# Kernel tuning notes

Hardware: AMD Instinct MI355X
Metric: run time of the kernel (lower is better)

## Reference

```python
import jax, jax.numpy as jnp
import numpy as np

B, N, FDIM, REL, H = 4, 256, 256, 16, 8
D = FDIM // H


def setup_inputs() -> dict:
    key = jax.random.key(0)
    ks = jax.random.split(key, 10)
    s_f = 1.0 / np.sqrt(FDIM)
    s_kv = 1.0 / np.sqrt(FDIM + REL)
    return {
        "node_features": jax.random.normal(ks[0], (B, N, FDIM), jnp.float32),
        "relative_positions": jax.random.normal(ks[1], (B, N, N, REL), jnp.float32),
        # torch Linear weights stored transposed -> here [in, out]
        "Wq": jax.random.uniform(ks[2], (FDIM, FDIM), jnp.float32, -s_f, s_f),
        "bq": jax.random.uniform(ks[3], (FDIM,), jnp.float32, -s_f, s_f),
        "Wk": jax.random.uniform(ks[4], (FDIM + REL, FDIM), jnp.float32, -s_kv, s_kv),
        "bk": jax.random.uniform(ks[5], (FDIM,), jnp.float32, -s_kv, s_kv),
        "Wv": jax.random.uniform(ks[6], (FDIM + REL, FDIM), jnp.float32, -s_kv, s_kv),
        "bv": jax.random.uniform(ks[7], (FDIM,), jnp.float32, -s_kv, s_kv),
        "Wo": jax.random.uniform(ks[8], (FDIM, FDIM), jnp.float32, -s_f, s_f),
        "bo": jax.random.uniform(ks[9], (FDIM,), jnp.float32, -s_f, s_f),
    }


def reference(node_features, relative_positions, Wq, bq, Wk, bk, Wv, bv, Wo, bo):
    b, n, f = node_features.shape
    # Q: [b, n_i, H, D]
    Q = (node_features @ Wq + bq).reshape(b, n, H, D)
    # per-edge K/V input: [b, i, j, f+rel] where feature part is node j's features
    nf_j = jnp.broadcast_to(node_features[:, None, :, :], (b, n, n, f))
    kv_in = jnp.concatenate([nf_j, relative_positions], axis=-1)
    K = (kv_in @ Wk + bk).reshape(b, n, n, H, D)  # [b, i, j, h, d]
    V = (kv_in @ Wv + bv).reshape(b, n, n, H, D)
    scale = 1.0 / jnp.sqrt(jnp.asarray(D, node_features.dtype))
    scores = jnp.einsum('bihd,bijhd->bhij', Q, K) * scale
    attn = jax.nn.softmax(scores, axis=-1)
    wv = jnp.einsum('bhij,bijhd->bihd', attn, V).reshape(b, n, f)
    return node_features + (wv @ Wo + bo)
```

## Files before the change

kernel.cpp:

```cpp
#include <hip/hip_runtime.h>


#define BB 4
#define NN 256
#define FD 256
#define RL 16
#define NH 8
#define HD 32

#define OFF_Q    0
#define OFF_KN   (BB*NN*FD)
#define OFF_VN   (OFF_KN + BB*NN*FD/2)

#define ATP 260
#define RLP 20

static __device__ __forceinline__ unsigned short f2bf(float x) {
  unsigned int u = __float_as_uint(x);
  unsigned int r = (u + 0x7fffu + ((u >> 16) & 1u)) >> 16;
  return (unsigned short)r;
}
static __device__ __forceinline__ float bf2f(unsigned short h) {
  return __uint_as_float(((unsigned int)h) << 16);
}
static __device__ __forceinline__ float4 bf4(ushort4 u) {
  return make_float4(bf2f(u.x), bf2f(u.y), bf2f(u.z), bf2f(u.w));
}

__global__ __launch_bounds__(256) void k_qkv5(
    const float* __restrict__ nf,
    const float* __restrict__ Wq, const float* __restrict__ bq,
    const float* __restrict__ Wk, const float* __restrict__ bk,
    const float* __restrict__ Wv, const float* __restrict__ bv,
    float* __restrict__ ws) {
  const int ROWS = 8;
  __shared__ float lrowT[FD][ROWS];
  const int row0 = blockIdx.x * ROWS;
  const int sel  = blockIdx.y;
  const float* W; const float* bias;
  if (sel == 0)      { W = Wq; bias = bq; }
  else if (sel == 1) { W = Wk; bias = bk; }
  else               { W = Wv; bias = bv; }
  const int tid = threadIdx.x;
  {
    float v[ROWS];
    #pragma unroll
    for (int t = 0; t < ROWS; ++t) v[t] = nf[(row0 + t) * FD + tid];
    #pragma unroll
    for (int t = 0; t < ROWS; ++t) lrowT[tid][t] = v[t];
  }
  __syncthreads();
  float acc[ROWS];
  #pragma unroll
  for (int r = 0; r < ROWS; ++r) acc[r] = 0.f;
  #pragma unroll 8
  for (int k = 0; k < FD; ++k) {
    const float w = W[k * FD + tid];
    float4 a0 = *(const float4*)&lrowT[k][0];
    float4 a1 = *(const float4*)&lrowT[k][4];
    acc[0] += a0.x * w; acc[1] += a0.y * w; acc[2] += a0.z * w; acc[3] += a0.w * w;
    acc[4] += a1.x * w; acc[5] += a1.y * w; acc[6] += a1.z * w; acc[7] += a1.w * w;
  }
  const float bb = bias[tid];
  if (sel == 1) {
    const int b2 = row0 >> 8, i0 = row0 & 255;
    unsigned short* kout = (unsigned short*)(ws + OFF_KN) + ((size_t)b2 * FD + tid) * NN + i0;
    ushort4 v0, v1;
    v0.x = f2bf(acc[0] + bb); v0.y = f2bf(acc[1] + bb);
    v0.z = f2bf(acc[2] + bb); v0.w = f2bf(acc[3] + bb);
    v1.x = f2bf(acc[4] + bb); v1.y = f2bf(acc[5] + bb);
    v1.z = f2bf(acc[6] + bb); v1.w = f2bf(acc[7] + bb);
    ((ushort4*)kout)[0] = v0;
    ((ushort4*)kout)[1] = v1;
  } else if (sel == 2) {
    unsigned short* outp = (unsigned short*)(ws + OFF_VN);
    #pragma unroll
    for (int r = 0; r < ROWS; ++r)
      outp[(size_t)(row0 + r) * FD + tid] = f2bf(acc[r] + bb);
  } else {
    float* outp = ws + OFF_Q;
    #pragma unroll
    for (int r = 0; r < ROWS; ++r)
      outp[(row0 + r) * FD + tid] = acc[r] + bb;
  }
}

__global__ __launch_bounds__(256, 2) void k_attn5(
    const float* __restrict__ rel,
    const float* __restrict__ Wk,
    const float* __restrict__ Wv,
    const float* __restrict__ nf,
    const float* __restrict__ Wo,
    const float* __restrict__ bo,
    float* __restrict__ out,
    float* __restrict__ ws) {
  const float* Q = ws + OFF_Q;
  const unsigned short* KnB = (const unsigned short*)(ws + OFF_KN);
  const unsigned short* VnB = (const unsigned short*)(ws + OFF_VN);

  const int bid = (blockIdx.x & 7) * 64 + (blockIdx.x >> 3);
  const int b  = bid >> 7;
  const int i0 = (bid & 127) * 2;
  const int tid = threadIdx.x;
  const int l = tid & 63, w = tid >> 6;

  __shared__ float q[2][FD];
  __shared__ float qrs[2][NH * RL];
  __shared__ float rlds[2 * NN * RLP];
  __shared__ float at[2 * NH * ATP];
  __shared__ float ar[2][NH * RL];
  __shared__ float part[8 * FD];
  __shared__ float wvT[FD * 2];

  const float scale = 0.17677669529663687f;
  q[0][tid] = Q[(b * NN + i0) * FD + tid] * scale;
  q[1][tid] = Q[(b * NN + i0 + 1) * FD + tid] * scale;

  #pragma unroll
  for (int ii = 0; ii < 2; ++ii) {
    const float4* rp = (const float4*)(rel + ((size_t)(b * NN + i0 + ii)) * (NN * RL));
    #pragma unroll
    for (int m = 0; m < 4; ++m) {
      const int idx = tid + 256 * m;
      float4 v = rp[idx];
      *(float4*)&rlds[(ii * NN + (idx >> 2)) * RLP + (idx & 3) * 4] = v;
    }
  }

  {
    const int ii = l >> 5, hh = (l >> 4) & 1, r = l & 15;
    const int h = 2 * w + hh;
    const float* wrow = Wk + (FD + r) * FD + h * HD;
    const float* qq = &q[ii][h * HD];
    float a = 0.f;
    #pragma unroll
    for (int d = 0; d < HD; ++d) a += qq[d] * wrow[d];
    qrs[ii][h * RL + r] = a;
  }
  __syncthreads();

  float s[2][2][4];
  #pragma unroll
  for (int ii = 0; ii < 2; ++ii)
    #pragma unroll
    for (int hh = 0; hh < 2; ++hh)
      #pragma unroll
      for (int jj = 0; jj < 4; ++jj) s[ii][hh][jj] = 0.f;
  {
    const ushort4* kp = (const ushort4*)(KnB + ((size_t)b * FD + 64 * w) * NN) + l;
    #pragma unroll 2
    for (int dd = 0; dd < 8; ++dd) {
      float4 qv00 = *(const float4*)&q[0][64 * w + 4 * dd];
      float4 qv01 = *(const float4*)&q[0][64 * w + 32 + 4 * dd];
      float4 qv10 = *(const float4*)&q[1][64 * w + 4 * dd];
      float4 qv11 = *(const float4*)&q[1][64 * w + 32 + 4 * dd];
      #pragma unroll
      for (int e = 0; e < 4; ++e) {
        float4 k0 = bf4(kp[(4 * dd + e) * (NN / 4)]);
        float4 k1 = bf4(kp[(32 + 4 * dd + e) * (NN / 4)]);
        const float a0 = (&qv00.x)[e], a1 = (&qv01.x)[e];
        const float b0 = (&qv10.x)[e], b1 = (&qv11.x)[e];
        s[0][0][0] += a0 * k0.x; s[0][0][1] += a0 * k0.y;
        s[0][0][2] += a0 * k0.z; s[0][0][3] += a0 * k0.w;
        s[1][0][0] += b0 * k0.x; s[1][0][1] += b0 * k0.y;
        s[1][0][2] += b0 * k0.z; s[1][0][3] += b0 * k0.w;
        s[0][1][0] += a1 * k1.x; s[0][1][1] += a1 * k1.y;
        s[0][1][2] += a1 * k1.z; s[0][1][3] += a1 * k1.w;
        s[1][1][0] += b1 * k1.x; s[1][1][1] += b1 * k1.y;
        s[1][1][2] += b1 * k1.z; s[1][1][3] += b1 * k1.w;
      }
    }
  }

  #pragma unroll
  for (int ii = 0; ii < 2; ++ii) {
    float4 qa0 = *(const float4*)&qrs[ii][(2 * w) * RL + 0];
    float4 qa1 = *(const float4*)&qrs[ii][(2 * w) * RL + 4];
    float4 qa2 = *(const float4*)&qrs[ii][(2 * w) * RL + 8];
    float4 qa3 = *(const float4*)&qrs[ii][(2 * w) * RL + 12];
    float4 qb0 = *(const float4*)&qrs[ii][(2 * w + 1) * RL + 0];
    float4 qb1 = *(const float4*)&qrs[ii][(2 * w + 1) * RL + 4];
    float4 qb2 = *(const float4*)&qrs[ii][(2 * w + 1) * RL + 8];
    float4 qb3 = *(const float4*)&qrs[ii][(2 * w + 1) * RL + 12];
    #pragma unroll
    for (int jj = 0; jj < 4; ++jj) {
      const float* rv = &rlds[(ii * NN + 4 * l + jj) * RLP];
      float4 r0 = *(const float4*)&rv[0];
      float4 r1 = *(const float4*)&rv[4];
      float4 r2 = *(const float4*)&rv[8];
      float4 r3 = *(const float4*)&rv[12];
      s[ii][0][jj] += qa0.x*r0.x + qa0.y*r0.y + qa0.z*r0.z + qa0.w*r0.w
                    + qa1.x*r1.x + qa1.y*r1.y + qa1.z*r1.z + qa1.w*r1.w
                    + qa2.x*r2.x + qa2.y*r2.y + qa2.z*r2.z + qa2.w*r2.w
                    + qa3.x*r3.x + qa3.y*r3.y + qa3.z*r3.z + qa3.w*r3.w;
      s[ii][1][jj] += qb0.x*r0.x + qb0.y*r0.y + qb0.z*r0.z + qb0.w*r0.w
                    + qb1.x*r1.x + qb1.y*r1.y + qb1.z*r1.z + qb1.w*r1.w
                    + qb2.x*r2.x + qb2.y*r2.y + qb2.z*r2.z + qb2.w*r2.w
                    + qb3.x*r3.x + qb3.y*r3.y + qb3.z*r3.z + qb3.w*r3.w;
    }
  }

  #pragma unroll
  for (int ii = 0; ii < 2; ++ii) {
    #pragma unroll
    for (int hh = 0; hh < 2; ++hh) {
      float v = fmaxf(fmaxf(s[ii][hh][0], s[ii][hh][1]),
                      fmaxf(s[ii][hh][2], s[ii][hh][3]));
      #pragma unroll
      for (int off = 32; off; off >>= 1) v = fmaxf(v, __shfl_xor(v, off));
      float4 p;
      p.x = __expf(s[ii][hh][0] - v); p.y = __expf(s[ii][hh][1] - v);
      p.z = __expf(s[ii][hh][2] - v); p.w = __expf(s[ii][hh][3] - v);
      float sum = p.x + p.y + p.z + p.w;
      #pragma unroll
      for (int off = 32; off; off >>= 1) sum += __shfl_xor(sum, off);
      const float rec = 1.f / sum;
      p.x *= rec; p.y *= rec; p.z *= rec; p.w *= rec;
      *(float4*)&at[(ii * NH + 2 * w + hh) * ATP + 4 * l] = p;
    }
  }

  #pragma unroll
  for (int ii = 0; ii < 2; ++ii) {
    const int r = l & 15, sl = l >> 4;
    const int h = 2 * w + (sl & 1);
    const int jb = (sl >> 1) * 128;
    const float* atp = at + (ii * NH + h) * ATP + jb;
    const float* rlp = rlds + (ii * NN + jb) * RLP + r;
    float a = 0.f;
    #pragma unroll 4
    for (int jj = 0; jj < 128; ++jj) a += atp[jj] * rlp[jj * RLP];
    a += __shfl_xor(a, 32);
    if (l < 32) ar[ii][32 * w + l] = a;
  }
  __syncthreads();

  {
    const int h = l >> 3;
    const ushort4* vp = (const ushort4*)(VnB + (size_t)b * NN * FD) + l;
    const float* ap0 = at + h * ATP + 64 * w;
    const float* ap1 = at + (NH + h) * ATP + 64 * w;
    float4 a0 = make_float4(0,0,0,0), a1 = make_float4(0,0,0,0);
    #pragma unroll 4
    for (int jj = 0; jj < 64; ++jj) {
      float4 v = bf4(vp[(64 * w + jj) * (FD / 4)]);
      float p0 = ap0[jj], p1 = ap1[jj];
      a0.x += p0*v.x; a0.y += p0*v.y; a0.z += p0*v.z; a0.w += p0*v.w;
      a1.x += p1*v.x; a1.y += p1*v.y; a1.z += p1*v.z; a1.w += p1*v.w;
    }
    ((float4*)part)[w * 64 + l]       = a0;
    ((float4*)part)[(4 + w) * 64 + l] = a1;
  }
  __syncthreads();

  {
    const int c = tid, h2 = c >> 5;
    float s0 = part[c] + part[FD + c] + part[2*FD + c] + part[3*FD + c];
    float s1 = part[4*FD + c] + part[5*FD + c] + part[6*FD + c] + part[7*FD + c];
    #pragma unroll
    for (int r = 0; r < RL; ++r) {
      const float wvr = Wv[(FD + r) * FD + c];
      s0 += ar[0][h2 * RL + r] * wvr;
      s1 += ar[1][h2 * RL + r] * wvr;
    }
    *(float2*)&wvT[2 * c] = make_float2(s0, s1);
  }
  __syncthreads();

  {
    const int c = tid;
    float acc0 = 0.f, acc1 = 0.f;
    #pragma unroll 4
    for (int k4 = 0; k4 < FD / 4; ++k4) {
      float4 wa = *(const float4*)&wvT[8 * k4];
      float4 wb = *(const float4*)&wvT[8 * k4 + 4];
      float w0 = Wo[(4 * k4 + 0) * FD + c];
      float w1 = Wo[(4 * k4 + 1) * FD + c];
      float w2 = Wo[(4 * k4 + 2) * FD + c];
      float w3 = Wo[(4 * k4 + 3) * FD + c];
      acc0 += wa.x * w0 + wa.z * w1 + wb.x * w2 + wb.z * w3;
      acc1 += wa.y * w0 + wa.w * w1 + wb.y * w2 + wb.w * w3;
    }
    const float bb = bo[c];
    out[(b * NN + i0) * FD + c]     = nf[(b * NN + i0) * FD + c]     + acc0 + bb;
    out[(b * NN + i0 + 1) * FD + c] = nf[(b * NN + i0 + 1) * FD + c] + acc1 + bb;
  }
}

extern "C" void kernel_launch(void* const* d_in, const int* in_sizes, int n_in,
                              void* d_out, int out_size, void* d_ws, size_t ws_size,
                              hipStream_t stream) {
  const float* nf  = (const float*)d_in[0];
  const float* rel = (const float*)d_in[1];
  const float* Wq  = (const float*)d_in[2];
  const float* bq  = (const float*)d_in[3];
  const float* Wk  = (const float*)d_in[4];
  const float* bk  = (const float*)d_in[5];
  const float* Wv  = (const float*)d_in[6];
  const float* bv  = (const float*)d_in[7];
  const float* Wo  = (const float*)d_in[8];
  const float* bo  = (const float*)d_in[9];
  float* out = (float*)d_out;
  float* ws  = (float*)d_ws;

  k_qkv5 <<<dim3(BB * NN / 8, 3), 256, 0, stream>>>(nf, Wq, bq, Wk, bk, Wv, bv, ws);
  k_attn5<<<BB * NN / 2, 256, 0, stream>>>(rel, Wk, Wv, nf, Wo, bo, out, ws);
}
```

Measured before the change: 41.61 us.

## Double threads per block, split-K QKV projection, transpose rel layout, bf16 Wo

```diff
diff --git a/kernel.cpp b/kernel.cpp
--- a/kernel.cpp
+++ b/kernel.cpp
@@ -11,9 +11,10 @@
 #define OFF_Q    0
 #define OFF_KN   (BB*NN*FD)
 #define OFF_VN   (OFF_KN + BB*NN*FD/2)
+#define OFF_WO   (OFF_VN + BB*NN*FD/2)
 
 #define ATP 260
-#define RLP 20
+#define RLT 262
 
 static __device__ __forceinline__ unsigned short f2bf(float x) {
   unsigned int u = __float_as_uint(x);
@@ -23,80 +24,101 @@
 static __device__ __forceinline__ float bf2f(unsigned short h) {
   return __uint_as_float(((unsigned int)h) << 16);
 }
-static __device__ __forceinline__ float4 bf4(ushort4 u) {
-  return make_float4(bf2f(u.x), bf2f(u.y), bf2f(u.z), bf2f(u.w));
-}
-
-__global__ __launch_bounds__(256) void k_qkv5(
+
+__global__ __launch_bounds__(512) void k_qkv6(
     const float* __restrict__ nf,
     const float* __restrict__ Wq, const float* __restrict__ bq,
     const float* __restrict__ Wk, const float* __restrict__ bk,
     const float* __restrict__ Wv, const float* __restrict__ bv,
+    const float* __restrict__ Wo,
     float* __restrict__ ws) {
-  const int ROWS = 8;
-  __shared__ float lrowT[FD][ROWS];
-  const int row0 = blockIdx.x * ROWS;
-  const int sel  = blockIdx.y;
+  const int tid = threadIdx.x;
+  const int sel = blockIdx.y;
+  if (sel == 3) {
+    if (tid < 256) {
+      const int k2 = blockIdx.x;
+      unsigned int lo = f2bf(Wo[(2 * k2) * FD + tid]);
+      unsigned int hi = f2bf(Wo[(2 * k2 + 1) * FD + tid]);
+      ((unsigned int*)(ws + OFF_WO))[k2 * FD + tid] = lo | (hi << 16);
+    }
+    return;
+  }
+  __shared__ __align__(16) float lrowT[FD * 12];
+  const int row0 = blockIdx.x * 8;
   const float* W; const float* bias;
   if (sel == 0)      { W = Wq; bias = bq; }
   else if (sel == 1) { W = Wk; bias = bk; }
   else               { W = Wv; bias = bv; }
-  const int tid = threadIdx.x;
-  {
-    float v[ROWS];
-    #pragma unroll
-    for (int t = 0; t < ROWS; ++t) v[t] = nf[(row0 + t) * FD + tid];
-    #pragma unroll
-    for (int t = 0; t < ROWS; ++t) lrowT[tid][t] = v[t];
-  }
-  __syncthreads();
-  float acc[ROWS];
-  #pragma unroll
-  for (int r = 0; r < ROWS; ++r) acc[r] = 0.f;
-  #pragma unroll 8
-  for (int k = 0; k < FD; ++k) {
-    const float w = W[k * FD + tid];
-    float4 a0 = *(const float4*)&lrowT[k][0];
-    float4 a1 = *(const float4*)&lrowT[k][4];
-    acc[0] += a0.x * w; acc[1] += a0.y * w; acc[2] += a0.z * w; acc[3] += a0.w * w;
-    acc[4] += a1.x * w; acc[5] += a1.y * w; acc[6] += a1.z * w; acc[7] += a1.w * w;
-  }
-  const float bb = bias[tid];
-  if (sel == 1) {
-    const int b2 = row0 >> 8, i0 = row0 & 255;
-    unsigned short* kout = (unsigned short*)(ws + OFF_KN) + ((size_t)b2 * FD + tid) * NN + i0;
-    ushort4 v0, v1;
-    v0.x = f2bf(acc[0] + bb); v0.y = f2bf(acc[1] + bb);
-    v0.z = f2bf(acc[2] + bb); v0.w = f2bf(acc[3] + bb);
-    v1.x = f2bf(acc[4] + bb); v1.y = f2bf(acc[5] + bb);
-    v1.z = f2bf(acc[6] + bb); v1.w = f2bf(acc[7] + bb);
-    ((ushort4*)kout)[0] = v0;
-    ((ushort4*)kout)[1] = v1;
-  } else if (sel == 2) {
-    unsigned short* outp = (unsigned short*)(ws + OFF_VN);
-    #pragma unroll
-    for (int r = 0; r < ROWS; ++r)
-      outp[(size_t)(row0 + r) * FD + tid] = f2bf(acc[r] + bb);
-  } else {
-    float* outp = ws + OFF_Q;
-    #pragma unroll
-    for (int r = 0; r < ROWS; ++r)
-      outp[(row0 + r) * FD + tid] = acc[r] + bb;
-  }
-}
-
-__global__ __launch_bounds__(256, 2) void k_attn5(
+  #pragma unroll
+  for (int t = 0; t < 4; ++t) {
+    int idx = tid + t * 512;
+    int k = idx & 255, r = idx >> 8;
+    lrowT[k * 12 + r] = nf[(row0 + r) * FD + k];
+  }
+  __syncthreads();
+  const int col = tid & 255, half = tid >> 8;
+  float acc[8];
+  #pragma unroll
+  for (int r = 0; r < 8; ++r) acc[r] = 0.f;
+  {
+    const float* Wp = W + (half * 128) * FD + col;
+    const float* lp = lrowT + (half * 128) * 12;
+    #pragma unroll 8
+    for (int kk = 0; kk < 128; ++kk) {
+      const float w = Wp[kk * FD];
+      float4 a0 = *(const float4*)&lp[kk * 12];
+      float4 a1 = *(const float4*)&lp[kk * 12 + 4];
+      acc[0] += a0.x * w; acc[1] += a0.y * w; acc[2] += a0.z * w; acc[3] += a0.w * w;
+      acc[4] += a1.x * w; acc[5] += a1.y * w; acc[6] += a1.z * w; acc[7] += a1.w * w;
+    }
+  }
+  __syncthreads();
+  float* red = lrowT;
+  if (half) {
+    #pragma unroll
+    for (int r = 0; r < 8; ++r) red[r * 256 + col] = acc[r];
+  }
+  __syncthreads();
+  if (!half) {
+    #pragma unroll
+    for (int r = 0; r < 8; ++r) acc[r] += red[r * 256 + col];
+    const float bb = bias[col];
+    if (sel == 1) {
+      const int b2 = row0 >> 8, i0 = row0 & 255;
+      unsigned short* kout = (unsigned short*)(ws + OFF_KN) + ((size_t)b2 * FD + col) * NN + i0;
+      ushort4 v0, v1;
+      v0.x = f2bf(acc[0] + bb); v0.y = f2bf(acc[1] + bb);
+      v0.z = f2bf(acc[2] + bb); v0.w = f2bf(acc[3] + bb);
+      v1.x = f2bf(acc[4] + bb); v1.y = f2bf(acc[5] + bb);
+      v1.z = f2bf(acc[6] + bb); v1.w = f2bf(acc[7] + bb);
+      ((ushort4*)kout)[0] = v0;
+      ((ushort4*)kout)[1] = v1;
+    } else if (sel == 2) {
+      unsigned short* outp = (unsigned short*)(ws + OFF_VN);
+      #pragma unroll
+      for (int r = 0; r < 8; ++r)
+        outp[(size_t)(row0 + r) * FD + col] = f2bf(acc[r] + bb);
+    } else {
+      float* outp = ws + OFF_Q;
+      #pragma unroll
+      for (int r = 0; r < 8; ++r)
+        outp[(row0 + r) * FD + col] = acc[r] + bb;
+    }
+  }
+}
+
+__global__ __launch_bounds__(512, 1) void k_attn6(
     const float* __restrict__ rel,
     const float* __restrict__ Wk,
     const float* __restrict__ Wv,
     const float* __restrict__ nf,
-    const float* __restrict__ Wo,
     const float* __restrict__ bo,
     float* __restrict__ out,
     float* __restrict__ ws) {
   const float* Q = ws + OFF_Q;
   const unsigned short* KnB = (const unsigned short*)(ws + OFF_KN);
   const unsigned short* VnB = (const unsigned short*)(ws + OFF_VN);
+  const unsigned int* WoP = (const unsigned int*)(ws + OFF_WO);
 
   const int bid = (blockIdx.x & 7) * 64 + (blockIdx.x >> 3);
   const int b  = bid >> 7;
@@ -106,30 +128,32 @@
 
   __shared__ float q[2][FD];
   __shared__ float qrs[2][NH * RL];
-  __shared__ float rlds[2 * NN * RLP];
+  __shared__ __align__(16) float rldsT[2 * RL * RLT];
   __shared__ float at[2 * NH * ATP];
   __shared__ float ar[2][NH * RL];
-  __shared__ float part[8 * FD];
-  __shared__ float wvT[FD * 2];
+  float* part = rldsT;
+  float* wvT  = rldsT + 16 * 256;
 
   const float scale = 0.17677669529663687f;
-  q[0][tid] = Q[(b * NN + i0) * FD + tid] * scale;
-  q[1][tid] = Q[(b * NN + i0 + 1) * FD + tid] * scale;
-
-  #pragma unroll
-  for (int ii = 0; ii < 2; ++ii) {
+  q[tid >> 8][tid & 255] = Q[(b * NN + i0 + (tid >> 8)) * FD + (tid & 255)] * scale;
+
+  {
+    const int ii = w >> 2, q4 = w & 3;
     const float4* rp = (const float4*)(rel + ((size_t)(b * NN + i0 + ii)) * (NN * RL));
     #pragma unroll
     for (int m = 0; m < 4; ++m) {
-      const int idx = tid + 256 * m;
-      float4 v = rp[idx];
-      *(float4*)&rlds[(ii * NN + (idx >> 2)) * RLP + (idx & 3) * 4] = v;
-    }
-  }
-
-  {
-    const int ii = l >> 5, hh = (l >> 4) & 1, r = l & 15;
-    const int h = 2 * w + hh;
+      const int j = l + 64 * m;
+      float4 v = rp[j * 4 + q4];
+      rldsT[(ii * RL + 4 * q4 + 0) * RLT + j] = v.x;
+      rldsT[(ii * RL + 4 * q4 + 1) * RLT + j] = v.y;
+      rldsT[(ii * RL + 4 * q4 + 2) * RLT + j] = v.z;
+      rldsT[(ii * RL + 4 * q4 + 3) * RLT + j] = v.w;
+    }
+  }
+  __syncthreads();
+
+  if (tid < 256) {
+    const int ii = tid >> 7, h = (tid >> 4) & 7, r = tid & 15;
     const float* wrow = Wk + (FD + r) * FD + h * HD;
     const float* qq = &q[ii][h * HD];
     float a = 0.f;
@@ -137,153 +161,117 @@
     for (int d = 0; d < HD; ++d) a += qq[d] * wrow[d];
     qrs[ii][h * RL + r] = a;
   }
-  __syncthreads();
-
-  float s[2][2][4];
-  #pragma unroll
-  for (int ii = 0; ii < 2; ++ii)
-    #pragma unroll
-    for (int hh = 0; hh < 2; ++hh)
-      #pragma unroll
-      for (int jj = 0; jj < 4; ++jj) s[ii][hh][jj] = 0.f;
-  {
-    const ushort4* kp = (const ushort4*)(KnB + ((size_t)b * FD + 64 * w) * NN) + l;
-    #pragma unroll 2
-    for (int dd = 0; dd < 8; ++dd) {
-      float4 qv00 = *(const float4*)&q[0][64 * w + 4 * dd];
-      float4 qv01 = *(const float4*)&q[0][64 * w + 32 + 4 * dd];
-      float4 qv10 = *(const float4*)&q[1][64 * w + 4 * dd];
-      float4 qv11 = *(const float4*)&q[1][64 * w + 32 + 4 * dd];
-      #pragma unroll
-      for (int e = 0; e < 4; ++e) {
-        float4 k0 = bf4(kp[(4 * dd + e) * (NN / 4)]);
-        float4 k1 = bf4(kp[(32 + 4 * dd + e) * (NN / 4)]);
-        const float a0 = (&qv00.x)[e], a1 = (&qv01.x)[e];
-        const float b0 = (&qv10.x)[e], b1 = (&qv11.x)[e];
-        s[0][0][0] += a0 * k0.x; s[0][0][1] += a0 * k0.y;
-        s[0][0][2] += a0 * k0.z; s[0][0][3] += a0 * k0.w;
-        s[1][0][0] += b0 * k0.x; s[1][0][1] += b0 * k0.y;
-        s[1][0][2] += b0 * k0.z; s[1][0][3] += b0 * k0.w;
-        s[0][1][0] += a1 * k1.x; s[0][1][1] += a1 * k1.y;
-        s[0][1][2] += a1 * k1.z; s[0][1][3] += a1 * k1.w;
-        s[1][1][0] += b1 * k1.x; s[1][1][1] += b1 * k1.y;
-        s[1][1][2] += b1 * k1.z; s[1][1][3] += b1 * k1.w;
-      }
-    }
-  }
+
+  float s[2][4] = {{0.f,0.f,0.f,0.f},{0.f,0.f,0.f,0.f}};
+  {
+    const ushort2* krow = (const ushort2*)(KnB + ((size_t)b * FD + w * HD) * NN);
+    const float* q0 = &q[0][w * HD];
+    const float* q1 = &q[1][w * HD];
+    #pragma unroll 4
+    for (int d = 0; d < HD; ++d) {
+      ushort2 ua = krow[d * 128 + l];
+      ushort2 ub = krow[d * 128 + 64 + l];
+      float k0 = bf2f(ua.x), k1 = bf2f(ua.y), k2 = bf2f(ub.x), k3 = bf2f(ub.y);
+      float qa = q0[d], qb = q1[d];
+      s[0][0] += qa * k0; s[0][1] += qa * k1; s[0][2] += qa * k2; s[0][3] += qa * k3;
+      s[1][0] += qb * k0; s[1][1] += qb * k1; s[1][2] += qb * k2; s[1][3] += qb * k3;
+    }
+  }
+  __syncthreads();
 
   #pragma unroll
   for (int ii = 0; ii < 2; ++ii) {
-    float4 qa0 = *(const float4*)&qrs[ii][(2 * w) * RL + 0];
-    float4 qa1 = *(const float4*)&qrs[ii][(2 * w) * RL + 4];
-    float4 qa2 = *(const float4*)&qrs[ii][(2 * w) * RL + 8];
-    float4 qa3 = *(const float4*)&qrs[ii][(2 * w) * RL + 12];
-    float4 qb0 = *(const float4*)&qrs[ii][(2 * w + 1) * RL + 0];
-    float4 qb1 = *(const float4*)&qrs[ii][(2 * w + 1) * RL + 4];
-    float4 qb2 = *(const float4*)&qrs[ii][(2 * w + 1) * RL + 8];
-    float4 qb3 = *(const float4*)&qrs[ii][(2 * w + 1) * RL + 12];
-    #pragma unroll
-    for (int jj = 0; jj < 4; ++jj) {
-      const float* rv = &rlds[(ii * NN + 4 * l + jj) * RLP];
-      float4 r0 = *(const float4*)&rv[0];
-      float4 r1 = *(const float4*)&rv[4];
-      float4 r2 = *(const float4*)&rv[8];
-      float4 r3 = *(const float4*)&rv[12];
-      s[ii][0][jj] += qa0.x*r0.x + qa0.y*r0.y + qa0.z*r0.z + qa0.w*r0.w
-                    + qa1.x*r1.x + qa1.y*r1.y + qa1.z*r1.z + qa1.w*r1.w
-                    + qa2.x*r2.x + qa2.y*r2.y + qa2.z*r2.z + qa2.w*r2.w
-                    + qa3.x*r3.x + qa3.y*r3.y + qa3.z*r3.z + qa3.w*r3.w;
-      s[ii][1][jj] += qb0.x*r0.x + qb0.y*r0.y + qb0.z*r0.z + qb0.w*r0.w
-                    + qb1.x*r1.x + qb1.y*r1.y + qb1.z*r1.z + qb1.w*r1.w
-                    + qb2.x*r2.x + qb2.y*r2.y + qb2.z*r2.z + qb2.w*r2.w
-                    + qb3.x*r3.x + qb3.y*r3.y + qb3.z*r3.z + qb3.w*r3.w;
+    #pragma unroll
+    for (int r = 0; r < RL; ++r) {
+      const float qv = qrs[ii][w * RL + r];
+      const float* rr = &rldsT[(ii * RL + r) * RLT];
+      float2 ra = *(const float2*)&rr[2 * l];
+      float2 rb = *(const float2*)&rr[2 * l + 128];
+      s[ii][0] += qv * ra.x; s[ii][1] += qv * ra.y;
+      s[ii][2] += qv * rb.x; s[ii][3] += qv * rb.y;
     }
   }
 
   #pragma unroll
   for (int ii = 0; ii < 2; ++ii) {
-    #pragma unroll
-    for (int hh = 0; hh < 2; ++hh) {
-      float v = fmaxf(fmaxf(s[ii][hh][0], s[ii][hh][1]),
-                      fmaxf(s[ii][hh][2], s[ii][hh][3]));
-      #pragma unroll
-      for (int off = 32; off; off >>= 1) v = fmaxf(v, __shfl_xor(v, off));
-      float4 p;
-      p.x = __expf(s[ii][hh][0] - v); p.y = __expf(s[ii][hh][1] - v);
-      p.z = __expf(s[ii][hh][2] - v); p.w = __expf(s[ii][hh][3] - v);
-      float sum = p.x + p.y + p.z + p.w;
-      #pragma unroll
-      for (int off = 32; off; off >>= 1) sum += __shfl_xor(sum, off);
-      const float rec = 1.f / sum;
-      p.x *= rec; p.y *= rec; p.z *= rec; p.w *= rec;
-      *(float4*)&at[(ii * NH + 2 * w + hh) * ATP + 4 * l] = p;
-    }
+    float v = fmaxf(fmaxf(s[ii][0], s[ii][1]), fmaxf(s[ii][2], s[ii][3]));
+    #pragma unroll
+    for (int off = 32; off; off >>= 1) v = fmaxf(v, __shfl_xor(v, off));
+    float p0 = __expf(s[ii][0] - v), p1 = __expf(s[ii][1] - v);
+    float p2 = __expf(s[ii][2] - v), p3 = __expf(s[ii][3] - v);
+    float sum = p0 + p1 + p2 + p3;
+    #pragma unroll
+    for (int off = 32; off; off >>= 1) sum += __shfl_xor(sum, off);
+    const float rec = 1.f / sum;
+    *(float2*)&at[(ii * NH + w) * ATP + 2 * l]       = make_float2(p0 * rec, p1 * rec);
+    *(float2*)&at[(ii * NH + w) * ATP + 2 * l + 128] = make_float2(p2 * rec, p3 * rec);
   }
 
   #pragma unroll
   for (int ii = 0; ii < 2; ++ii) {
-    const int r = l & 15, sl = l >> 4;
-    const int h = 2 * w + (sl & 1);
-    const int jb = (sl >> 1) * 128;
-    const float* atp = at + (ii * NH + h) * ATP + jb;
-    const float* rlp = rlds + (ii * NN + jb) * RLP + r;
+    const int r = l & 15, q4 = l >> 4;
+    const float* arow = &at[(ii * NH + w) * ATP];
+    const float* rrow = &rldsT[(ii * RL + r) * RLT];
     float a = 0.f;
     #pragma unroll 4
-    for (int jj = 0; jj < 128; ++jj) a += atp[jj] * rlp[jj * RLP];
+    for (int jj = 0; jj < 64; ++jj) {
+      const int j = 4 * jj + q4;
+      a += arow[j] * rrow[j];
+    }
+    a += __shfl_xor(a, 16);
     a += __shfl_xor(a, 32);
-    if (l < 32) ar[ii][32 * w + l] = a;
-  }
-  __syncthreads();
-
-  {
-    const int h = l >> 3;
-    const ushort4* vp = (const ushort4*)(VnB + (size_t)b * NN * FD) + l;
-    const float* ap0 = at + h * ATP + 64 * w;
-    const float* ap1 = at + (NH + h) * ATP + 64 * w;
-    float4 a0 = make_float4(0,0,0,0), a1 = make_float4(0,0,0,0);
+    if (l < 16) ar[ii][w * RL + l] = a;
+  }
+  __syncthreads();
+
+  {
+    const int h = l >> 4;
+    const ushort2* vrow = (const ushort2*)(VnB + (size_t)b * NN * FD);
+    float a00=0.f,a01=0.f,a02=0.f,a03=0.f, a10=0.f,a11=0.f,a12=0.f,a13=0.f;
     #pragma unroll 4
-    for (int jj = 0; jj < 64; ++jj) {
-      float4 v = bf4(vp[(64 * w + jj) * (FD / 4)]);
-      float p0 = ap0[jj], p1 = ap1[jj];
-      a0.x += p0*v.x; a0.y += p0*v.y; a0.z += p0*v.z; a0.w += p0*v.w;
-      a1.x += p1*v.x; a1.y += p1*v.y; a1.z += p1*v.z; a1.w += p1*v.w;
-    }
-    ((float4*)part)[w * 64 + l]       = a0;
-    ((float4*)part)[(4 + w) * 64 + l] = a1;
-  }
-  __syncthreads();
-
-  {
-    const int c = tid, h2 = c >> 5;
-    float s0 = part[c] + part[FD + c] + part[2*FD + c] + part[3*FD + c];
-    float s1 = part[4*FD + c] + part[5*FD + c] + part[6*FD + c] + part[7*FD + c];
-    #pragma unroll
-    for (int r = 0; r < RL; ++r) {
-      const float wvr = Wv[(FD + r) * FD + c];
-      s0 += ar[0][h2 * RL + r] * wvr;
-      s1 += ar[1][h2 * RL + r] * wvr;
-    }
-    *(float2*)&wvT[2 * c] = make_float2(s0, s1);
-  }
-  __syncthreads();
-
-  {
-    const int c = tid;
-    float acc0 = 0.f, acc1 = 0.f;
-    #pragma unroll 4
-    for (int k4 = 0; k4 < FD / 4; ++k4) {
-      float4 wa = *(const float4*)&wvT[8 * k4];
-      float4 wb = *(const float4*)&wvT[8 * k4 + 4];
-      float w0 = Wo[(4 * k4 + 0) * FD + c];
-      float w1 = Wo[(4 * k4 + 1) * FD + c];
-      float w2 = Wo[(4 * k4 + 2) * FD + c];
-      float w3 = Wo[(4 * k4 + 3) * FD + c];
-      acc0 += wa.x * w0 + wa.z * w1 + wb.x * w2 + wb.z * w3;
-      acc1 += wa.y * w0 + wa.w * w1 + wb.y * w2 + wb.w * w3;
-    }
-    const float bb = bo[c];
-    out[(b * NN + i0) * FD + c]     = nf[(b * NN + i0) * FD + c]     + acc0 + bb;
-    out[(b * NN + i0 + 1) * FD + c] = nf[(b * NN + i0 + 1) * FD + c] + acc1 + bb;
+    for (int jj = 0; jj < 32; ++jj) {
+      const int j = 32 * w + jj;
+      ushort2 ua = vrow[j * 128 + l];
+      ushort2 ub = vrow[j * 128 + 64 + l];
+      float v0 = bf2f(ua.x), v1 = bf2f(ua.y), v2 = bf2f(ub.x), v3 = bf2f(ub.y);
+      float p0  = at[h * ATP + j];
+      float p0b = at[(h + 4) * ATP + j];
+      float p1  = at[(NH + h) * ATP + j];
+      float p1b = at[(NH + h + 4) * ATP + j];
+      a00 += p0 * v0;  a01 += p0 * v1;  a02 += p0b * v2; a03 += p0b * v3;
+      a10 += p1 * v0;  a11 += p1 * v1;  a12 += p1b * v2; a13 += p1b * v3;
+    }
+    *(float2*)&part[(0 * NH + w) * 256 + 2 * l]       = make_float2(a00, a01);
+    *(float2*)&part[(0 * NH + w) * 256 + 2 * l + 128] = make_float2(a02, a03);
+    *(float2*)&part[(1 * NH + w) * 256 + 2 * l]       = make_float2(a10, a11);
+    *(float2*)&part[(1 * NH + w) * 256 + 2 * l + 128] = make_float2(a12, a13);
+  }
+  __syncthreads();
+
+  {
+    const int ii = tid >> 8, c = tid & 255, h2 = c >> 5;
+    float sE = 0.f;
+    #pragma unroll
+    for (int w2 = 0; w2 < 8; ++w2) sE += part[(ii * NH + w2) * 256 + c];
+    #pragma unroll
+    for (int r = 0; r < RL; ++r)
+      sE += ar[ii][h2 * RL + r] * Wv[(FD + r) * FD + c];
+    wvT[c * 2 + ii] = sE;
+  }
+  __syncthreads();
+
+  {
+    const int ii = tid >> 8, c = tid & 255;
+    float acc = 0.f;
+    #pragma unroll 8
+    for (int k2 = 0; k2 < 128; ++k2) {
+      unsigned int u = WoP[k2 * FD + c];
+      float w0 = bf2f((unsigned short)(u & 0xffffu));
+      float w1 = bf2f((unsigned short)(u >> 16));
+      acc += wvT[(2 * k2) * 2 + ii] * w0 + wvT[(2 * k2 + 1) * 2 + ii] * w1;
+    }
+    const int row = b * NN + i0 + ii;
+    out[row * FD + c] = nf[row * FD + c] + acc + bo[c];
   }
 }
 
@@ -303,6 +291,6 @@
   float* out = (float*)d_out;
   float* ws  = (float*)d_ws;
 
-  k_qkv5 <<<dim3(BB * NN / 8, 3), 256, 0, stream>>>(nf, Wq, bq, Wk, bk, Wv, bv, ws);
-  k_attn5<<<BB * NN / 2, 256, 0, stream>>>(rel, Wk, Wv, nf, Wo, bo, out, ws);
-}
+  k_qkv6 <<<dim3(BB * NN / 8, 4), 512, 0, stream>>>(nf, Wq, bq, Wk, bk, Wv, bv, Wo, ws);
+  k_attn6<<<BB * NN / 2, 512, 0, stream>>>(rel, Wk, Wv, nf, bo, out, ws);
+}
```

After: 43.00 us. 1.03x slower.

## Shrink LDS with bf16 transposed rel tile, prepack Wo to bf16, raise occupancy

Applied to the files above, without the earlier changes.

```diff
diff --git a/kernel.cpp b/kernel.cpp
--- a/kernel.cpp
+++ b/kernel.cpp
@@ -11,9 +11,10 @@
 #define OFF_Q    0
 #define OFF_KN   (BB*NN*FD)
 #define OFF_VN   (OFF_KN + BB*NN*FD/2)
+#define OFF_WO   (OFF_VN + BB*NN*FD/2)
 
 #define ATP 260
-#define RLP 20
+#define RLT 130
 
 static __device__ __forceinline__ unsigned short f2bf(float x) {
   unsigned int u = __float_as_uint(x);
@@ -23,55 +24,51 @@
 static __device__ __forceinline__ float bf2f(unsigned short h) {
   return __uint_as_float(((unsigned int)h) << 16);
 }
-static __device__ __forceinline__ float4 bf4(ushort4 u) {
-  return make_float4(bf2f(u.x), bf2f(u.y), bf2f(u.z), bf2f(u.w));
-}
-
-__global__ __launch_bounds__(256) void k_qkv5(
+
+__global__ __launch_bounds__(256, 4) void k_qkv9(
     const float* __restrict__ nf,
     const float* __restrict__ Wq, const float* __restrict__ bq,
     const float* __restrict__ Wk, const float* __restrict__ bk,
     const float* __restrict__ Wv, const float* __restrict__ bv,
+    const float* __restrict__ Wo,
     float* __restrict__ ws) {
-  const int ROWS = 8;
+  const int tid = threadIdx.x;
+  const int sel = blockIdx.y;
+  if (sel == 3) {
+    if (blockIdx.x < 128) {
+      const int k2 = blockIdx.x;
+      unsigned int lo = f2bf(Wo[(2 * k2) * FD + tid]);
+      unsigned int hi = f2bf(Wo[(2 * k2 + 1) * FD + tid]);
+      ((unsigned int*)(ws + OFF_WO))[k2 * FD + tid] = lo | (hi << 16);
+    }
+    return;
+  }
+  const int ROWS = 4;
   __shared__ float lrowT[FD][ROWS];
   const int row0 = blockIdx.x * ROWS;
-  const int sel  = blockIdx.y;
   const float* W; const float* bias;
   if (sel == 0)      { W = Wq; bias = bq; }
   else if (sel == 1) { W = Wk; bias = bk; }
   else               { W = Wv; bias = bv; }
-  const int tid = threadIdx.x;
-  {
-    float v[ROWS];
-    #pragma unroll
-    for (int t = 0; t < ROWS; ++t) v[t] = nf[(row0 + t) * FD + tid];
-    #pragma unroll
-    for (int t = 0; t < ROWS; ++t) lrowT[tid][t] = v[t];
-  }
-  __syncthreads();
-  float acc[ROWS];
-  #pragma unroll
-  for (int r = 0; r < ROWS; ++r) acc[r] = 0.f;
-  #pragma unroll 8
+  #pragma unroll
+  for (int t = 0; t < ROWS; ++t)
+    lrowT[tid][t] = nf[(row0 + t) * FD + tid];
+  __syncthreads();
+  float acc[ROWS] = {0.f, 0.f, 0.f, 0.f};
+  #pragma unroll 16
   for (int k = 0; k < FD; ++k) {
     const float w = W[k * FD + tid];
     float4 a0 = *(const float4*)&lrowT[k][0];
-    float4 a1 = *(const float4*)&lrowT[k][4];
     acc[0] += a0.x * w; acc[1] += a0.y * w; acc[2] += a0.z * w; acc[3] += a0.w * w;
-    acc[4] += a1.x * w; acc[5] += a1.y * w; acc[6] += a1.z * w; acc[7] += a1.w * w;
   }
   const float bb = bias[tid];
   if (sel == 1) {
     const int b2 = row0 >> 8, i0 = row0 & 255;
     unsigned short* kout = (unsigned short*)(ws + OFF_KN) + ((size_t)b2 * FD + tid) * NN + i0;
-    ushort4 v0, v1;
+    ushort4 v0;
     v0.x = f2bf(acc[0] + bb); v0.y = f2bf(acc[1] + bb);
     v0.z = f2bf(acc[2] + bb); v0.w = f2bf(acc[3] + bb);
-    v1.x = f2bf(acc[4] + bb); v1.y = f2bf(acc[5] + bb);
-    v1.z = f2bf(acc[6] + bb); v1.w = f2bf(acc[7] + bb);
-    ((ushort4*)kout)[0] = v0;
-    ((ushort4*)kout)[1] = v1;
+    *((ushort4*)kout) = v0;
   } else if (sel == 2) {
     unsigned short* outp = (unsigned short*)(ws + OFF_VN);
     #pragma unroll
@@ -85,18 +82,18 @@
   }
 }
 
-__global__ __launch_bounds__(256, 2) void k_attn5(
+__global__ __launch_bounds__(256, 4) void k_attn9(
     const float* __restrict__ rel,
     const float* __restrict__ Wk,
     const float* __restrict__ Wv,
     const float* __restrict__ nf,
-    const float* __restrict__ Wo,
     const float* __restrict__ bo,
     float* __restrict__ out,
     float* __restrict__ ws) {
   const float* Q = ws + OFF_Q;
   const unsigned short* KnB = (const unsigned short*)(ws + OFF_KN);
   const unsigned short* VnB = (const unsigned short*)(ws + OFF_VN);
+  const unsigned int* WoP = (const unsigned int*)(ws + OFF_WO);
 
   const int bid = (blockIdx.x & 7) * 64 + (blockIdx.x >> 3);
   const int b  = bid >> 7;
@@ -106,11 +103,11 @@
 
   __shared__ float q[2][FD];
   __shared__ float qrs[2][NH * RL];
-  __shared__ float rlds[2 * NN * RLP];
-  __shared__ float at[2 * NH * ATP];
   __shared__ float ar[2][NH * RL];
-  __shared__ float part[8 * FD];
-  __shared__ float wvT[FD * 2];
+  __shared__ __align__(16) float at[2 * NH * ATP];
+  __shared__ __align__(16) unsigned int rldsT[2 * RL * RLT];
+  float* part = (float*)rldsT;
+  float* wvT  = (float*)rldsT + 2048;
 
   const float scale = 0.17677669529663687f;
   q[0][tid] = Q[(b * NN + i0) * FD + tid] * scale;
@@ -120,10 +117,16 @@
   for (int ii = 0; ii < 2; ++ii) {
     const float4* rp = (const float4*)(rel + ((size_t)(b * NN + i0 + ii)) * (NN * RL));
     #pragma unroll
-    for (int m = 0; m < 4; ++m) {
-      const int idx = tid + 256 * m;
-      float4 v = rp[idx];
-      *(float4*)&rlds[(ii * NN + (idx >> 2)) * RLP + (idx & 3) * 4] = v;
+    for (int m = 0; m < 2; ++m) {
+      const int t = tid + 256 * m;
+      const int jp = t >> 2, q4 = t & 3;
+      float4 va = rp[8 * jp + q4];
+      float4 vb = rp[8 * jp + 4 + q4];
+      unsigned int* base = &rldsT[(ii * RL + 4 * q4) * RLT + jp];
+      base[0]       = (unsigned int)f2bf(va.x) | ((unsigned int)f2bf(vb.x) << 16);
+      base[RLT]     = (unsigned int)f2bf(va.y) | ((unsigned int)f2bf(vb.y) << 16);
+      base[2 * RLT] = (unsigned int)f2bf(va.z) | ((unsigned int)f2bf(vb.z) << 16);
+      base[3 * RLT] = (unsigned int)f2bf(va.w) | ((unsigned int)f2bf(vb.w) << 16);
     }
   }
 
@@ -156,8 +159,10 @@
       float4 qv11 = *(const float4*)&q[1][64 * w + 32 + 4 * dd];
       #pragma unroll
       for (int e = 0; e < 4; ++e) {
-        float4 k0 = bf4(kp[(4 * dd + e) * (NN / 4)]);
-        float4 k1 = bf4(kp[(32 + 4 * dd + e) * (NN / 4)]);
+        ushort4 u0 = kp[(4 * dd + e) * (NN / 4)];
+        ushort4 u1 = kp[(32 + 4 * dd + e) * (NN / 4)];
+        float4 k0 = make_float4(bf2f(u0.x), bf2f(u0.y), bf2f(u0.z), bf2f(u0.w));
+        float4 k1 = make_float4(bf2f(u1.x), bf2f(u1.y), bf2f(u1.z), bf2f(u1.w));
         const float a0 = (&qv00.x)[e], a1 = (&qv01.x)[e];
         const float b0 = (&qv10.x)[e], b1 = (&qv11.x)[e];
         s[0][0][0] += a0 * k0.x; s[0][0][1] += a0 * k0.y;
@@ -174,29 +179,19 @@
 
   #pragma unroll
   for (int ii = 0; ii < 2; ++ii) {
-    float4 qa0 = *(const float4*)&qrs[ii][(2 * w) * RL + 0];
-    float4 qa1 = *(const float4*)&qrs[ii][(2 * w) * RL + 4];
-    float4 qa2 = *(const float4*)&qrs[ii][(2 * w) * RL + 8];
-    float4 qa3 = *(const float4*)&qrs[ii][(2 * w) * RL + 12];
-    float4 qb0 = *(const float4*)&qrs[ii][(2 * w + 1) * RL + 0];
-    float4 qb1 = *(const float4*)&qrs[ii][(2 * w + 1) * RL + 4];
-    float4 qb2 = *(const float4*)&qrs[ii][(2 * w + 1) * RL + 8];
-    float4 qb3 = *(const float4*)&qrs[ii][(2 * w + 1) * RL + 12];
-    #pragma unroll
-    for (int jj = 0; jj < 4; ++jj) {
-      const float* rv = &rlds[(ii * NN + 4 * l + jj) * RLP];
-      float4 r0 = *(const float4*)&rv[0];
-      float4 r1 = *(const float4*)&rv[4];
-      float4 r2 = *(const float4*)&rv[8];
-      float4 r3 = *(const float4*)&rv[12];
-      s[ii][0][jj] += qa0.x*r0.x + qa0.y*r0.y + qa0.z*r0.z + qa0.w*r0.w
-                    + qa1.x*r1.x + qa1.y*r1.y + qa1.z*r1.z + qa1.w*r1.w
-                    + qa2.x*r2.x + qa2.y*r2.y + qa2.z*r2.z + qa2.w*r2.w
-                    + qa3.x*r3.x + qa3.y*r3.y + qa3.z*r3.z + qa3.w*r3.w;
-      s[ii][1][jj] += qb0.x*r0.x + qb0.y*r0.y + qb0.z*r0.z + qb0.w*r0.w
-                    + qb1.x*r1.x + qb1.y*r1.y + qb1.z*r1.z + qb1.w*r1.w
-                    + qb2.x*r2.x + qb2.y*r2.y + qb2.z*r2.z + qb2.w*r2.w
-                    + qb3.x*r3.x + qb3.y*r3.y + qb3.z*r3.z + qb3.w*r3.w;
+    #pragma unroll
+    for (int r = 0; r < RL; ++r) {
+      uint2 u = *(const uint2*)&rldsT[(ii * RL + r) * RLT + 2 * l];
+      float r0 = bf2f((unsigned short)(u.x & 0xffffu));
+      float r1 = bf2f((unsigned short)(u.x >> 16));
+      float r2 = bf2f((unsigned short)(u.y & 0xffffu));
+      float r3 = bf2f((unsigned short)(u.y >> 16));
+      const float qa = qrs[ii][(2 * w) * RL + r];
+      const float qb = qrs[ii][(2 * w + 1) * RL + r];
+      s[ii][0][0] += qa * r0; s[ii][0][1] += qa * r1;
+      s[ii][0][2] += qa * r2; s[ii][0][3] += qa * r3;
+      s[ii][1][0] += qb * r0; s[ii][1][1] += qb * r1;
+      s[ii][1][2] += qb * r2; s[ii][1][3] += qb * r3;
     }
   }
 
@@ -226,10 +221,14 @@
     const int h = 2 * w + (sl & 1);
     const int jb = (sl >> 1) * 128;
     const float* atp = at + (ii * NH + h) * ATP + jb;
-    const float* rlp = rlds + (ii * NN + jb) * RLP + r;
+    const unsigned int* rr_ = &rldsT[(ii * RL + r) * RLT + (jb >> 1)];
     float a = 0.f;
-    #pragma unroll 4
-    for (int jj = 0; jj < 128; ++jj) a += atp[jj] * rlp[jj * RLP];
+    #pragma unroll 8
+    for (int u = 0; u < 64; ++u) {
+      unsigned int x = rr_[u];
+      a += atp[2 * u]     * bf2f((unsigned short)(x & 0xffffu));
+      a += atp[2 * u + 1] * bf2f((unsigned short)(x >> 16));
+    }
     a += __shfl_xor(a, 32);
     if (l < 32) ar[ii][32 * w + l] = a;
   }
@@ -243,7 +242,8 @@
     float4 a0 = make_float4(0,0,0,0), a1 = make_float4(0,0,0,0);
     #pragma unroll 4
     for (int jj = 0; jj < 64; ++jj) {
-      float4 v = bf4(vp[(64 * w + jj) * (FD / 4)]);
+      ushort4 u = vp[(64 * w + jj) * (FD / 4)];
+      float4 v = make_float4(bf2f(u.x), bf2f(u.y), bf2f(u.z), bf2f(u.w));
       float p0 = ap0[jj], p1 = ap1[jj];
       a0.x += p0*v.x; a0.y += p0*v.y; a0.z += p0*v.z; a0.w += p0*v.w;
       a1.x += p1*v.x; a1.y += p1*v.y; a1.z += p1*v.z; a1.w += p1*v.w;
@@ -270,20 +270,20 @@
   {
     const int c = tid;
     float acc0 = 0.f, acc1 = 0.f;
-    #pragma unroll 4
-    for (int k4 = 0; k4 < FD / 4; ++k4) {
-      float4 wa = *(const float4*)&wvT[8 * k4];
-      float4 wb = *(const float4*)&wvT[8 * k4 + 4];
-      float w0 = Wo[(4 * k4 + 0) * FD + c];
-      float w1 = Wo[(4 * k4 + 1) * FD + c];
-      float w2 = Wo[(4 * k4 + 2) * FD + c];
-      float w3 = Wo[(4 * k4 + 3) * FD + c];
-      acc0 += wa.x * w0 + wa.z * w1 + wb.x * w2 + wb.z * w3;
-      acc1 += wa.y * w0 + wa.w * w1 + wb.y * w2 + wb.w * w3;
+    #pragma unroll 8
+    for (int k2 = 0; k2 < 128; ++k2) {
+      unsigned int u = WoP[k2 * FD + c];
+      float w0 = bf2f((unsigned short)(u & 0xffffu));
+      float w1 = bf2f((unsigned short)(u >> 16));
+      float2 wa = *(const float2*)&wvT[4 * k2];
+      float2 wb = *(const float2*)&wvT[4 * k2 + 2];
+      acc0 += wa.x * w0 + wb.x * w1;
+      acc1 += wa.y * w0 + wb.y * w1;
     }
     const float bb = bo[c];
-    out[(b * NN + i0) * FD + c]     = nf[(b * NN + i0) * FD + c]     + acc0 + bb;
-    out[(b * NN + i0 + 1) * FD + c] = nf[(b * NN + i0 + 1) * FD + c] + acc1 + bb;
+    const int row = b * NN + i0;
+    out[row * FD + c]       = nf[row * FD + c]       + acc0 + bb;
+    out[(row + 1) * FD + c] = nf[(row + 1) * FD + c] + acc1 + bb;
   }
 }
 
@@ -303,6 +303,6 @@
   float* out = (float*)d_out;
   float* ws  = (float*)d_ws;
 
-  k_qkv5 <<<dim3(BB * NN / 8, 3), 256, 0, stream>>>(nf, Wq, bq, Wk, bk, Wv, bv, ws);
-  k_attn5<<<BB * NN / 2, 256, 0, stream>>>(rel, Wk, Wv, nf, Wo, bo, out, ws);
-}
+  k_qkv9 <<<dim3(BB * NN / 4, 4), 256, 0, stream>>>(nf, Wq, bq, Wk, bk, Wv, bv, Wo, ws);
+  k_attn9<<<BB * NN / 2, 256, 0, stream>>>(rel, Wk, Wv, nf, bo, out, ws);
+}
```

Result: slower. 43.40 us (+4.3%).
